# Kernel optimization log

Hardware: AMD Instinct MI355X
Metric: run time of the kernel (lower is better)

Reference implementation:

```python
import jax, jax.numpy as jnp
import numpy as np


def setup_inputs() -> dict:
    key = jax.random.key(0)
    k1, k2, k3 = jax.random.split(key, 3)
    B, N, D = 8, 4096, 64
    q = jax.random.normal(k1, (B, N, D), dtype=jnp.float32)
    k = jax.random.normal(k2, (B, N, D), dtype=jnp.float32)
    v = jax.random.normal(k3, (B, N, D), dtype=jnp.float32)
    attn_mask = jnp.ones((B, N), dtype=jnp.int32)  # 1 = attend, 0 = padding
    return {"q": q, "k": k, "v": v, "attn_mask": attn_mask}


def reference(q, k, v, attn_mask):
    # q: [B, n_q, d], k/v: [B, n_k, d], attn_mask: [B, n_k]
    d = q.shape[-1]
    n_q, n_k = q.shape[1], k.shape[1]
    scale = jnp.sqrt(jnp.asarray(d, dtype=q.dtype))
    # [B, n_q, n_k] attention logits
    logits = jnp.einsum("bqd,bkd->bqk", q, k) / scale
    # causal (mask_future=True): tril keep-mask over (n_q, n_k)
    causal = jnp.tril(jnp.ones((n_q, n_k), dtype=bool))
    neg_inf = jnp.asarray(-jnp.inf, dtype=logits.dtype)
    logits = jnp.where(causal[None, :, :], logits, neg_inf)
    # padding mask broadcast over query dim: [B, 1, n_k]
    logits = jnp.where(attn_mask[:, None, :] == 0, neg_inf, logits)
    w = jax.nn.softmax(logits, axis=-1)
    return jnp.einsum("bqk,bkd->bqd", w, v)
```

## Files before the change

### kernel.cpp

```cpp
#include <hip/hip_runtime.h>


#define BATCH 8
#define SEQ   4096
#define DIM   64
#define QT    64
#define NKT   (SEQ / 64)

typedef __attribute__((ext_vector_type(8))) short bf16x8;
typedef __attribute__((ext_vector_type(4))) float f32x4;
typedef __attribute__((ext_vector_type(4))) unsigned u32x4;

__device__ inline short f2bf(float f) {
    unsigned u = __builtin_bit_cast(unsigned, f);
    u += 0x7FFFu + ((u >> 16) & 1u);
    return (short)(u >> 16);
}

__device__ inline unsigned pk2bf(float a, float b) {
    unsigned ua = __builtin_bit_cast(unsigned, a) + 0x8000u;
    unsigned ub = __builtin_bit_cast(unsigned, b) + 0x8000u;
    return __builtin_amdgcn_perm(ub, ua, 0x07060302u);
}

__device__ inline float fast_exp2(float x) {
#if __has_builtin(__builtin_amdgcn_exp2f)
    return __builtin_amdgcn_exp2f(x);
#else
    return exp2f(x);
#endif
}

__device__ inline void gl_lds16(const void* g, void* l) {
    __builtin_amdgcn_global_load_lds(
        (const __attribute__((address_space(1))) void*)g,
        (__attribute__((address_space(3))) void*)l, 16, 0, 0);
}

__device__ inline f32x4 ntl4(const float* p) {
    return __builtin_nontemporal_load((const f32x4*)p);
}

__global__ __launch_bounds__(256)
void prep_kv(const float* __restrict__ kg, const float* __restrict__ vg,
             const int* __restrict__ mg, short* __restrict__ kw,
             short* __restrict__ vw, float* __restrict__ mf) {
    const int tile = blockIdx.x;
    const float* kp = kg + (size_t)tile * 64 * DIM;
    const float* vp = vg + (size_t)tile * 64 * DIM;
    short* ko = kw + (size_t)tile * 4096;
    short* vo = vw + (size_t)tile * 4096;
    const int t = threadIdx.x;
    if (mf && t < 64) {
        const int* mp = mg + (size_t)tile * 64;
        mf[(size_t)tile * 64 + t] = mp[t] ? 0.0f : -1e30f;
    }
#pragma unroll
    for (int i = 0; i < 4; ++i) {
        const int flat = i * 256 + t;
        const int key = flat >> 4, d0 = (flat & 15) * 4;
        const f32x4 kv = ntl4(kp + (size_t)key * DIM + d0);
        uint2 kpk;
        kpk.x = pk2bf(kv[0], kv[1]); kpk.y = pk2bf(kv[2], kv[3]);
        *(uint2*)(ko + (((d0 >> 3) << 6) + key) * 8 + (d0 & 7)) = kpk;
        const f32x4 vv = ntl4(vp + (size_t)key * DIM + d0);
        const int vcell = ((key >> 5) << 2) | ((key >> 2) & 3);
        const int vj    = (((key >> 4) & 1) << 2) | (key & 3);
        vo[((vcell << 6) + d0 + 0) * 8 + vj] = f2bf(vv[0]);
        vo[((vcell << 6) + d0 + 1) * 8 + vj] = f2bf(vv[1]);
        vo[((vcell << 6) + d0 + 2) * 8 + vj] = f2bf(vv[2]);
        vo[((vcell << 6) + d0 + 3) * 8 + vj] = f2bf(vv[3]);
    }
}

__global__ __launch_bounds__(512, 6)
void attn_split3(const float* __restrict__ qg, float* __restrict__ og,
                 const short* __restrict__ kw, const short* __restrict__ vw,
                 const float* __restrict__ mf, float* __restrict__ opart,
                 float* __restrict__ lpart) {
    __shared__ __align__(16) char smem[49152];
    short* KbS = (short*)smem;
    float* OX = (float*)smem;
    float* LB = (float*)(smem + 16384);

    const int t    = threadIdx.x;
    const int w    = t >> 6;
    const int L    = t & 63;
    const int c15  = L & 15;
    const int quad = L >> 4;
    const int qsub = w & 3;
    const int kh   = w >> 2;

    const int id  = blockIdx.x;
    const int b   = id & 7;
    const int r_  = id >> 3;
    const int j   = r_ & 31;
    const int ch  = r_ >> 5;
    const int nL  = 64 - j;
    const int qLt = 63 - j;

    const float* qp  = qg + (size_t)b * SEQ * DIM;
    const float* mb  = mf + (size_t)b * SEQ;
    const short* kwb = kw + (size_t)b * NKT * 4096;
    const short* vwb = vw + (size_t)b * NKT * 4096;
    float* osl = opart + (size_t)(b * 32 + j) * 8192;
    float* lsl = lpart + (size_t)(b * 32 + j) * 256;
    const float qscale = 0.125f * 1.44269504088896340736f;

    auto stage = [&](int bs, int kt) {
        const short* ks = kwb + (size_t)kt * 4096;
        const short* vs = vwb + (size_t)kt * 4096;
        const int off = w << 9;
        gl_lds16(ks + off + (L << 3), KbS + bs * 8192 + off);
        gl_lds16(vs + off + (L << 3), KbS + bs * 8192 + 4096 + off);
    };

    bf16x8 vones;
#pragma unroll
    for (int z = 0; z < 8; ++z) vones[z] = (short)0x3F80;

    int sqt[2], sk0[2], sk1[2], smode[2], sos[2], sls[2], nseg;
    sos[0] = sos[1] = 0; sls[0] = sls[1] = 0;
    if (ch == 0) {
        nseg = 1;
        sqt[0] = qLt; sk0[0] = 0;  sk1[0] = 22; smode[0] = 0; sls[0] = 0;
    } else if (ch == 1) {
        if (nL >= 44) {
            nseg = 1;
            sqt[0] = qLt; sk0[0] = 22; sk1[0] = 44; smode[0] = 1; sos[0] = 0; sls[0] = 1;
        } else {
            nseg = 2;
            sqt[0] = qLt; sk0[0] = 22; sk1[0] = nL;      smode[0] = 1; sos[0] = 0; sls[0] = 1;
            sqt[1] = j;   sk0[1] = 0;  sk1[1] = 44 - nL; smode[1] = 0; sls[1] = 3;
        }
    } else {
        if (nL > 44) {
            nseg = 2;
            sqt[0] = qLt; sk0[0] = 44; sk1[0] = nL;    smode[0] = 1; sos[0] = 1; sls[0] = 2;
            sqt[1] = j;   sk0[1] = 0;  sk1[1] = j + 1; smode[1] = 2;
        } else if (nL == 44) {
            nseg = 1;
            sqt[0] = j; sk0[0] = 0; sk1[0] = j + 1; smode[0] = 2;
        } else {
            nseg = 1;
            sqt[0] = j; sk0[0] = 44 - nL; sk1[0] = j + 1; smode[0] = 1; sos[0] = 1; sls[0] = 2;
        }
    }

    for (int seg = 0; seg < nseg; ++seg) {
        const int qt   = sqt[seg];
        const int kt0  = sk0[seg];
        const int kt1  = sk1[seg];
        const int mode = smode[seg];

        const int qbase = qt * QT;
        const int qrow  = qbase + qsub * 16 + c15;

        bf16x8 Qf[2];
#pragma unroll
        for (int c = 0; c < 2; ++c) {
            const float* src = qp + (size_t)qrow * DIM + c * 32 + quad * 8;
            float4 x = *(const float4*)(src);
            float4 y = *(const float4*)(src + 4);
            bf16x8 f;
            f[0] = f2bf(x.x * qscale); f[1] = f2bf(x.y * qscale);
            f[2] = f2bf(x.z * qscale); f[3] = f2bf(x.w * qscale);
            f[4] = f2bf(y.x * qscale); f[5] = f2bf(y.y * qscale);
            f[6] = f2bf(y.z * qscale); f[7] = f2bf(y.w * qscale);
            Qf[c] = f;
        }
        asm volatile("" ::: "memory");

        f32x4 lacc = (f32x4){0.f, 0.f, 0.f, 0.f};
        f32x4 Oacc[4];
#pragma unroll
        for (int nb = 0; nb < 4; ++nb) Oacc[nb] = (f32x4){0.f, 0.f, 0.f, 0.f};

        stage(0, kt0);
        if (kt0 + 1 < kt1) stage(1, kt0 + 1);

        int bi = 0, b2 = 2;
        const float* mrow = mb + (size_t)kt0 * 64 + (2 * kh) * 16 + quad * 4;

        for (int kt = kt0; kt < kt1; ++kt) {
            if (kt + 1 < kt1) {
                asm volatile("s_waitcnt vmcnt(2)" ::: "memory");
            } else {
                asm volatile("s_waitcnt vmcnt(0)" ::: "memory");
            }
            __builtin_amdgcn_s_barrier();
            asm volatile("" ::: "memory");

            const float4 ma0 = *(const float4*)(mrow);
            const float4 ma1 = *(const float4*)(mrow + 16);
            mrow += 64;
            asm volatile("" ::: "memory");
            if (kt + 2 < kt1) stage(b2, kt + 2);
            b2 = (b2 == 2) ? 0 : b2 + 1;

            const short* Kt = KbS + bi * 8192;
            const short* Vt = Kt + 4096;
            bi = (bi == 2) ? 0 : bi + 1;

            f32x4 sacc[2];
            sacc[0] = (f32x4){ma0.x, ma0.y, ma0.z, ma0.w};
            sacc[1] = (f32x4){ma1.x, ma1.y, ma1.z, ma1.w};
            __builtin_amdgcn_s_setprio(1);
#pragma unroll
            for (int c = 0; c < 2; ++c) {
#pragma unroll
                for (int i = 0; i < 2; ++i) {
                    bf16x8 kf = *(const bf16x8*)&Kt[(((quad + 4 * c) << 6) + (2 * kh + i) * 16 + c15) * 8];
                    sacc[i] = __builtin_amdgcn_mfma_f32_16x16x32_bf16(kf, Qf[c], sacc[i], 0, 0, 0);
                }
            }
            __builtin_amdgcn_s_setprio(0);

            const bool diag = (kt == qt);
            unsigned pu[4];
#pragma unroll
            for (int i = 0; i < 2; ++i) {
                float p[4];
#pragma unroll
                for (int r = 0; r < 4; ++r) {
                    float s = sacc[i][r];
                    if (diag) {
                        const int keyg = kt * 64 + (2 * kh + i) * 16 + quad * 4 + r;
                        if (keyg > qrow) s = -1e30f;
                    }
                    p[r] = fast_exp2(s);
                }
                pu[2 * i]     = pk2bf(p[0], p[1]);
                pu[2 * i + 1] = pk2bf(p[2], p[3]);
            }

            const bf16x8 pf = __builtin_bit_cast(bf16x8,
                (u32x4){pu[0], pu[1], pu[2], pu[3]});
            __builtin_amdgcn_s_setprio(1);
#pragma unroll
            for (int nb = 0; nb < 4; ++nb) {
                bf16x8 vf = *(const bf16x8*)&Vt[(((kh * 4 + quad) << 6) + nb * 16 + c15) * 8];
                Oacc[nb] = __builtin_amdgcn_mfma_f32_16x16x32_bf16(pf, vf, Oacc[nb], 0, 0, 0);
            }
            lacc = __builtin_amdgcn_mfma_f32_16x16x32_bf16(pf, vones, lacc, 0, 0, 0);
            __builtin_amdgcn_s_setprio(0);
        }

        __syncthreads();
        if (w >= 4) {
            const int g = w & 3;
#pragma unroll
            for (int r = 0; r < 4; ++r) {
                const int q = quad * 4 + r;
#pragma unroll
                for (int nb = 0; nb < 4; ++nb)
                    OX[(g * 16 + q) * 64 + nb * 16 + c15] = Oacc[nb][r];
            }
            if (c15 == 0) {
#pragma unroll
                for (int r = 0; r < 4; ++r)
                    LB[g * 16 + quad * 4 + r] = lacc[r];
            }
        }
        __syncthreads();
        if (w < 4) {
            float lt_[4], inv_[4];
#pragma unroll
            for (int r = 0; r < 4; ++r) {
                lt_[r]  = lacc[r] + LB[w * 16 + quad * 4 + r];
                inv_[r] = 1.0f / lt_[r];
            }
            float* dst = (mode == 1) ? osl + (size_t)sos[seg] * 4096
                                     : og + ((size_t)b * SEQ + qbase) * DIM;
            if (mode != 2 && c15 == 0) {
#pragma unroll
                for (int r = 0; r < 4; ++r)
                    lsl[sls[seg] * 64 + w * 16 + quad * 4 + r] = lt_[r];
            }
#pragma unroll
            for (int r = 0; r < 4; ++r) {
                const float ir = (mode == 2) ? inv_[r] : 1.0f;
                const int rl = w * 16 + quad * 4 + r;
#pragma unroll
                for (int nb = 0; nb < 4; ++nb)
                    dst[(size_t)rl * DIM + nb * 16 + c15] =
                        (Oacc[nb][r] + OX[rl * 64 + nb * 16 + c15]) * ir;
            }
        }
        __syncthreads();
    }
}

__global__ __launch_bounds__(256)
void merge3(float* __restrict__ og, const float* __restrict__ opart,
            const float* __restrict__ lpart) {
    const int id = blockIdx.x;
    const int b = id & 7, j = id >> 3;
    const int nL = 64 - j, qLt = 63 - j;
    const float* os = opart + (size_t)(b * 32 + j) * 8192;
    const float* ls = lpart + (size_t)(b * 32 + j) * 256;
    const int t = threadIdx.x;
    const bool hasC = (nL > 44);

    float* opL = og + ((size_t)b * SEQ + (size_t)qLt * 64) * DIM;
#pragma unroll
    for (int i = 0; i < 4; ++i) {
        const int flat = i * 256 + t;
        const int row = flat >> 4;
        const int c4  = (flat & 15) * 4;
        float l = ls[row] + ls[64 + row];
        if (hasC) l += ls[128 + row];
        const float inv = 1.0f / l;
        const float4 a  = *(const float4*)(opL + (size_t)row * DIM + c4);
        const float4 p0 = *(const float4*)(os + (size_t)row * 64 + c4);
        float4 r;
        if (hasC) {
            const float4 p1 = *(const float4*)(os + 4096 + (size_t)row * 64 + c4);
            r.x = (a.x + p0.x + p1.x) * inv;
            r.y = (a.y + p0.y + p1.y) * inv;
            r.z = (a.z + p0.z + p1.z) * inv;
            r.w = (a.w + p0.w + p1.w) * inv;
        } else {
            r.x = (a.x + p0.x) * inv;
            r.y = (a.y + p0.y) * inv;
            r.z = (a.z + p0.z) * inv;
            r.w = (a.w + p0.w) * inv;
        }
        *(float4*)(opL + (size_t)row * DIM + c4) = r;
    }

    if (nL < 44) {
        float* opS = og + ((size_t)b * SEQ + (size_t)j * 64) * DIM;
#pragma unroll
        for (int i = 0; i < 4; ++i) {
            const int flat = i * 256 + t;
            const int row = flat >> 4;
            const int c4  = (flat & 15) * 4;
            const float inv = 1.0f / (ls[192 + row] + ls[128 + row]);
            const float4 a  = *(const float4*)(opS + (size_t)row * DIM + c4);
            const float4 p1 = *(const float4*)(os + 4096 + (size_t)row * 64 + c4);
            float4 r;
            r.x = (a.x + p1.x) * inv;
            r.y = (a.y + p1.y) * inv;
            r.z = (a.z + p1.z) * inv;
            r.w = (a.w + p1.w) * inv;
            *(float4*)(opS + (size_t)row * DIM + c4) = r;
        }
    }
}

template <bool WS>
__global__ __launch_bounds__(512, 4)
void attn_fwd(const float* __restrict__ qg, const float* __restrict__ kg,
              const float* __restrict__ vg, const int* __restrict__ mg,
              float* __restrict__ og, const short* __restrict__ kw,
              const short* __restrict__ vw) {
    __shared__ __align__(16) char smem[59392];
    short* KbS = (short*)smem;
    short* VbS = (short*)(smem + 16384);
    float* Ml  = (float*)(smem + 43008);
    float* OX = (float*)smem;
    float* LB = (float*)(smem + 16384);

    const int t    = threadIdx.x;
    const int w    = t >> 6;
    const int L    = t & 63;
    const int c15  = L & 15;
    const int quad = L >> 4;
    const int qsub = w & 3;
    const int kh   = w >> 2;

    const int id = blockIdx.x;
    const int b  = id & 7;
    const int j  = id >> 3;
    const int qb = (j < 32) ? (63 - j) : (j - 32);
    const int qbase  = qb * QT;
    const int ntiles = qb + 1;

    const float* qp = qg + (size_t)b * SEQ * DIM;
    const float* kp = kg + (size_t)b * SEQ * DIM;
    const float* vp = vg + (size_t)b * SEQ * DIM;
    const int*   mp = mg + (size_t)b * SEQ;
    const short* kwb = WS ? kw + (size_t)b * NKT * 4096 : nullptr;
    const short* vwb = WS ? vw + (size_t)b * NKT * 4096 : nullptr;

    const int qrow = qbase + qsub * 16 + c15;
    const float qscale = 0.125f * 1.44269504088896340736f;

    bf16x8 Qf[2];
#pragma unroll
    for (int c = 0; c < 2; ++c) {
        const float* src = qp + (size_t)qrow * DIM + c * 32 + quad * 8;
        float4 x = *(const float4*)(src);
        float4 y = *(const float4*)(src + 4);
        bf16x8 f;
        f[0] = f2bf(x.x * qscale); f[1] = f2bf(x.y * qscale);
        f[2] = f2bf(x.z * qscale); f[3] = f2bf(x.w * qscale);
        f[4] = f2bf(y.x * qscale); f[5] = f2bf(y.y * qscale);
        f[6] = f2bf(y.z * qscale); f[7] = f2bf(y.w * qscale);
        Qf[c] = f;
    }

    auto stage = [&](int bs, int kt) {
        const short* ks = kwb + (size_t)kt * 4096;
        const short* vs = vwb + (size_t)kt * 4096;
        const int off = w << 9;
        gl_lds16(ks + off + (L << 3), KbS + bs * 4096 + off);
        gl_lds16(vs + off + (L << 3), VbS + bs * 4096 + off);
    };

    for (int i = t; i < ntiles * 64; i += 512)
        Ml[i] = mp[i] ? 0.0f : -1e30f;

    float lsum = 0.0f;
    f32x4 Oacc[4];
#pragma unroll
    for (int nb = 0; nb < 4; ++nb) Oacc[nb] = (f32x4){0.f, 0.f, 0.f, 0.f};

    if constexpr (WS) stage(0, 0);

    for (int kt = 0; kt < ntiles; ++kt) {
        const int cur = WS ? (kt & 1) : 0;

        if constexpr (!WS) {
            __syncthreads();
#pragma unroll
            for (int it = 0; it < 2; ++it) {
                const int flat = it * 512 + t;
                const int key = flat >> 4, d0 = (flat & 15) * 4;
                const float4 kv = *(const float4*)(kp + (size_t)(kt * 64 + key) * DIM + d0);
                uint2 kk;
                kk.x = pk2bf(kv.x, kv.y); kk.y = pk2bf(kv.z, kv.w);
                *(uint2*)&KbS[(((d0 >> 3) << 6) + key) * 8 + (d0 & 7)] = kk;
                const float4 vv = *(const float4*)(vp + (size_t)(kt * 64 + key) * DIM + d0);
                const int vcell = ((key >> 5) << 2) | ((key >> 2) & 3);
                const int vj    = (((key >> 4) & 1) << 2) | (key & 3);
                VbS[((vcell << 6) + d0 + 0) * 8 + vj] = f2bf(vv.x);
                VbS[((vcell << 6) + d0 + 1) * 8 + vj] = f2bf(vv.y);
                VbS[((vcell << 6) + d0 + 2) * 8 + vj] = f2bf(vv.z);
                VbS[((vcell << 6) + d0 + 3) * 8 + vj] = f2bf(vv.w);
            }
            __syncthreads();
        } else {
            __syncthreads();
            if (kt + 1 < ntiles) stage(cur ^ 1, kt + 1);
        }

        const short* Kt = KbS + cur * 4096;
        const short* Vt = VbS + cur * 4096;

        f32x4 sacc[2];
        sacc[0] = (f32x4){0.f, 0.f, 0.f, 0.f};
        sacc[1] = (f32x4){0.f, 0.f, 0.f, 0.f};
#pragma unroll
        for (int c = 0; c < 2; ++c) {
#pragma unroll
            for (int i = 0; i < 2; ++i) {
                bf16x8 kf = *(const bf16x8*)&Kt[(((quad + 4 * c) << 6) + (2 * kh + i) * 16 + c15) * 8];
                sacc[i] = __builtin_amdgcn_mfma_f32_16x16x32_bf16(kf, Qf[c], sacc[i], 0, 0, 0);
            }
        }

        const bool diag = (kt == ntiles - 1);
        unsigned pu[4];
#pragma unroll
        for (int i = 0; i < 2; ++i) {
            const int kb = 2 * kh + i;
            const float4 ma = *(const float4*)&Ml[kt * 64 + kb * 16 + quad * 4];
            const float mar[4] = {ma.x, ma.y, ma.z, ma.w};
            float p[4];
#pragma unroll
            for (int r = 0; r < 4; ++r) {
                float s = sacc[i][r] + mar[r];
                if (diag) {
                    const int keyg = kt * 64 + kb * 16 + quad * 4 + r;
                    if (keyg > qrow) s = -1e30f;
                }
                p[r] = fast_exp2(fminf(s, 80.0f));
                lsum += p[r];
            }
            pu[2 * i]     = pk2bf(p[0], p[1]);
            pu[2 * i + 1] = pk2bf(p[2], p[3]);
        }

        const bf16x8 pf = __builtin_bit_cast(bf16x8,
            (u32x4){pu[0], pu[1], pu[2], pu[3]});
#pragma unroll
        for (int nb = 0; nb < 4; ++nb) {
            bf16x8 vf = *(const bf16x8*)&Vt[(((kh * 4 + quad) << 6) + nb * 16 + c15) * 8];
            Oacc[nb] = __builtin_amdgcn_mfma_f32_16x16x32_bf16(pf, vf, Oacc[nb], 0, 0, 0);
        }
    }

    lsum += __shfl_xor(lsum, 16);
    lsum += __shfl_xor(lsum, 32);

    __syncthreads();
    if (w >= 4) {
        const int g = w & 3;
#pragma unroll
        for (int r = 0; r < 4; ++r) {
            const int q = quad * 4 + r;
#pragma unroll
            for (int nb = 0; nb < 4; ++nb)
                OX[(g * 16 + q) * 64 + nb * 16 + c15] = Oacc[nb][r];
        }
        if (quad == 0) LB[g * 16 + c15] = lsum;
    }
    __syncthreads();
    if (w < 4) {
        const float inv = 1.0f / (lsum + LB[w * 16 + c15]);
        float* op = og + (size_t)b * SEQ * DIM;
#pragma unroll
        for (int r = 0; r < 4; ++r) {
            const float ir = __shfl(inv, (L & 48) + ((L & 48) >> 2) + r);
            const int row = qbase + w * 16 + quad * 4 + r;
#pragma unroll
            for (int nb = 0; nb < 4; ++nb)
                op[(size_t)row * DIM + nb * 16 + c15] =
                    (Oacc[nb][r] + OX[(w * 16 + quad * 4 + r) * 64 + nb * 16 + c15]) * ir;
        }
    }
}

extern "C" void kernel_launch(void* const* d_in, const int* in_sizes, int n_in,
                              void* d_out, int out_size, void* d_ws, size_t ws_size,
                              hipStream_t stream) {
    (void)in_sizes; (void)n_in; (void)out_size;
    const float* q = (const float*)d_in[0];
    const float* k = (const float*)d_in[1];
    const float* v = (const float*)d_in[2];
    const int*   m = (const int*)d_in[3];
    float* o = (float*)d_out;

    const size_t kvB    = (size_t)BATCH * NKT * 4096 * sizeof(short);
    const size_t maddB  = (size_t)BATCH * SEQ * sizeof(float);
    const size_t opartB = (size_t)BATCH * 32 * 8192 * sizeof(float);
    const size_t lpartB = (size_t)BATCH * 32 * 256 * sizeof(float);
    const size_t need3  = 2 * kvB + maddB + opartB + lpartB;

    if (ws_size >= need3) {
        short* kw = (short*)d_ws;
        short* vw = kw + (size_t)BATCH * NKT * 4096;
        float* mf = (float*)((char*)d_ws + 2 * kvB);
        float* opart = (float*)((char*)d_ws + 2 * kvB + maddB);
        float* lpart = opart + (size_t)BATCH * 32 * 8192;
        prep_kv<<<dim3(BATCH * NKT), 256, 0, stream>>>(k, v, m, kw, vw, mf);
        attn_split3<<<dim3(768), 512, 0, stream>>>(q, o, kw, vw, mf, opart, lpart);
        merge3<<<dim3(256), 256, 0, stream>>>(o, opart, lpart);
    } else if (ws_size >= 2 * kvB) {
        short* kw = (short*)d_ws;
        short* vw = kw + (size_t)BATCH * NKT * 4096;
        prep_kv<<<dim3(BATCH * NKT), 256, 0, stream>>>(k, v, m, kw, vw, nullptr);
        attn_fwd<true><<<dim3(512), 512, 0, stream>>>(q, k, v, m, o, kw, vw);
    } else {
        attn_fwd<false><<<dim3(512), 512, 0, stream>>>(q, k, v, m, o, nullptr, nullptr);
    }
}
```

Measured before the change: 119.3 us.

## Load K/V fragments directly from global memory instead of LDS triple buffering

Removes the async global-to-LDS triple-buffered staging of K and V tiles, along with the per-iteration barriers and waitcnt. Each wave now reads its bf16 K and V MFMA fragments straight from global memory (L2/cache) into registers, and LDS shrinks to just the final reduction buffers. This trades barrier synchronisation and LDS traffic for more global loads, since K/V are no longer shared across waves through LDS, and load latency is no longer hidden by explicit prefetch.

```diff
diff --git a/kernel.cpp b/kernel.cpp
--- a/kernel.cpp
+++ b/kernel.cpp
@@ -78,8 +78,7 @@
                  const short* __restrict__ kw, const short* __restrict__ vw,
                  const float* __restrict__ mf, float* __restrict__ opart,
                  float* __restrict__ lpart) {
-    __shared__ __align__(16) char smem[49152];
-    short* KbS = (short*)smem;
+    __shared__ __align__(16) char smem[16640];
     float* OX = (float*)smem;
     float* LB = (float*)(smem + 16384);
 
@@ -106,14 +105,6 @@
     float* osl = opart + (size_t)(b * 32 + j) * 8192;
     float* lsl = lpart + (size_t)(b * 32 + j) * 256;
     const float qscale = 0.125f * 1.44269504088896340736f;
-
-    auto stage = [&](int bs, int kt) {
-        const short* ks = kwb + (size_t)kt * 4096;
-        const short* vs = vwb + (size_t)kt * 4096;
-        const int off = w << 9;
-        gl_lds16(ks + off + (L << 3), KbS + bs * 8192 + off);
-        gl_lds16(vs + off + (L << 3), KbS + bs * 8192 + 4096 + off);
-    };
 
     bf16x8 vones;
 #pragma unroll
@@ -169,52 +160,46 @@
             f[6] = f2bf(y.z * qscale); f[7] = f2bf(y.w * qscale);
             Qf[c] = f;
         }
-        asm volatile("" ::: "memory");
 
         f32x4 lacc = (f32x4){0.f, 0.f, 0.f, 0.f};
         f32x4 Oacc[4];
 #pragma unroll
         for (int nb = 0; nb < 4; ++nb) Oacc[nb] = (f32x4){0.f, 0.f, 0.f, 0.f};
 
-        stage(0, kt0);
-        if (kt0 + 1 < kt1) stage(1, kt0 + 1);
-
-        int bi = 0, b2 = 2;
-        const float* mrow = mb + (size_t)kt0 * 64 + (2 * kh) * 16 + quad * 4;
+        const short* kbase = kwb + (size_t)kt0 * 4096;
+        const short* vbase = vwb + (size_t)kt0 * 4096;
+        const float* mrow  = mb + (size_t)kt0 * 64 + (2 * kh) * 16 + quad * 4;
 
         for (int kt = kt0; kt < kt1; ++kt) {
-            if (kt + 1 < kt1) {
-                asm volatile("s_waitcnt vmcnt(2)" ::: "memory");
-            } else {
-                asm volatile("s_waitcnt vmcnt(0)" ::: "memory");
-            }
-            __builtin_amdgcn_s_barrier();
-            asm volatile("" ::: "memory");
-
             const float4 ma0 = *(const float4*)(mrow);
             const float4 ma1 = *(const float4*)(mrow + 16);
             mrow += 64;
-            asm volatile("" ::: "memory");
-            if (kt + 2 < kt1) stage(b2, kt + 2);
-            b2 = (b2 == 2) ? 0 : b2 + 1;
-
-            const short* Kt = KbS + bi * 8192;
-            const short* Vt = Kt + 4096;
-            bi = (bi == 2) ? 0 : bi + 1;
+
+            bf16x8 kf[2][2];
+#pragma unroll
+            for (int c = 0; c < 2; ++c)
+#pragma unroll
+                for (int i = 0; i < 2; ++i)
+                    kf[c][i] = *(const bf16x8*)&kbase[(((quad + 4 * c) << 6) + (2 * kh + i) * 16 + c15) * 8];
 
             f32x4 sacc[2];
             sacc[0] = (f32x4){ma0.x, ma0.y, ma0.z, ma0.w};
             sacc[1] = (f32x4){ma1.x, ma1.y, ma1.z, ma1.w};
             __builtin_amdgcn_s_setprio(1);
 #pragma unroll
-            for (int c = 0; c < 2; ++c) {
-#pragma unroll
-                for (int i = 0; i < 2; ++i) {
-                    bf16x8 kf = *(const bf16x8*)&Kt[(((quad + 4 * c) << 6) + (2 * kh + i) * 16 + c15) * 8];
-                    sacc[i] = __builtin_amdgcn_mfma_f32_16x16x32_bf16(kf, Qf[c], sacc[i], 0, 0, 0);
-                }
-            }
+            for (int c = 0; c < 2; ++c)
+#pragma unroll
+                for (int i = 0; i < 2; ++i)
+                    sacc[i] = __builtin_amdgcn_mfma_f32_16x16x32_bf16(kf[c][i], Qf[c], sacc[i], 0, 0, 0);
             __builtin_amdgcn_s_setprio(0);
+
+            bf16x8 vf[4];
+#pragma unroll
+            for (int nb = 0; nb < 4; ++nb)
+                vf[nb] = *(const bf16x8*)&vbase[(((kh * 4 + quad) << 6) + nb * 16 + c15) * 8];
+
+            kbase += 4096;
+            vbase += 4096;
 
             const bool diag = (kt == qt);
             unsigned pu[4];
@@ -238,10 +223,8 @@
                 (u32x4){pu[0], pu[1], pu[2], pu[3]});
             __builtin_amdgcn_s_setprio(1);
 #pragma unroll
-            for (int nb = 0; nb < 4; ++nb) {
-                bf16x8 vf = *(const bf16x8*)&Vt[(((kh * 4 + quad) << 6) + nb * 16 + c15) * 8];
-                Oacc[nb] = __builtin_amdgcn_mfma_f32_16x16x32_bf16(pf, vf, Oacc[nb], 0, 0, 0);
-            }
+            for (int nb = 0; nb < 4; ++nb)
+                Oacc[nb] = __builtin_amdgcn_mfma_f32_16x16x32_bf16(pf, vf[nb], Oacc[nb], 0, 0, 0);
             lacc = __builtin_amdgcn_mfma_f32_16x16x32_bf16(pf, vones, lacc, 0, 0, 0);
             __builtin_amdgcn_s_setprio(0);
         }
```

Measured after the change: 138.0 us. +15.7%, slower.
